# Optimization experiments

Hardware: AMD Instinct MI355X
Metric: run time of the kernel (lower is better)

The kernel has to match this reference:

```python
import jax, jax.numpy as jnp
import numpy as np

B, D, O = 512, 512, 512  # batch, indim, outdim

def setup_inputs() -> dict:
    key = jax.random.key(0)
    k1, k2, k3 = jax.random.split(key, 3)
    x = jax.random.normal(k1, (B, D), dtype=jnp.float32)
    mu_weight = jax.random.normal(k2, (O, D), dtype=jnp.float32) / np.sqrt(D)
    # inverse diagonal covariance entries (positive in spirit; uniform fill)
    inv_diag_C_weight = jax.random.uniform(k3, (O, D), dtype=jnp.float32)
    return {"x": x, "mu_weight": mu_weight, "inv_diag_C_weight": inv_diag_C_weight}

def reference(x, mu_weight, inv_diag_C_weight):
    # Original: logits = -(x-mu) @ diag(invC) @ (x-mu)^T per (batch, class) pair.
    # Diagonal structure => elementwise squared diff weighted by invC, summed over D.
    diff = x[:, None, :] - mu_weight[None, :, :]            # [B, O, D]
    logits = -jnp.einsum('bod,od->bo', diff * diff, inv_diag_C_weight)
    return logits                                            # [B, O]
```

## Files before the change

### kernel.cpp

```cpp
#include <hip/hip_runtime.h>
#include <hip/hip_bf16.h>

#define B_DIM 512
#define D_DIM 512
#define O_DIM 512
#define DCH   128
#define NCH   (D_DIM/DCH)


typedef __attribute__((ext_vector_type(8))) short short8;
typedef __attribute__((ext_vector_type(4))) float f32x4;

__device__ __forceinline__ short f2bf(float f) {
    union { __hip_bfloat16 h; unsigned short u; } cv;
    cv.h = __float2bfloat16(f);
    return (short)cv.u;
}

__global__ __launch_bounds__(256)
void gda_mfma(const float* __restrict__ x,
              const float* __restrict__ mu,
              const float* __restrict__ ic,
              float* __restrict__ out)
{
    __shared__ unsigned short A_lds[32 * 256];
    __shared__ unsigned short B_lds[32 * 256];
    __shared__ float          c_part[32 * 8];
    __shared__ float          c_o[32];

    const int tid = threadIdx.x;
    const int bid = blockIdx.x;
    const int b0 = (bid & 15) * 32;
    const int o0 = (bid >> 4) * 32;

    const int srow = tid >> 3;
    const int su   = tid & 7;

    const int w    = tid >> 6;
    const int lane = tid & 63;
    const int wr   = w >> 1;
    const int wc   = w & 1;
    const int fcol = lane & 15;
    const int fk   = lane >> 4;

    const int rowA = wr * 16 + fcol;
    const int rowB = wc * 16 + fcol;
    const int swA7 = rowA & 7;
    const int swB7 = rowB & 7;

    float creg = 0.0f;
    f32x4 acc = {0.0f, 0.0f, 0.0f, 0.0f};

    for (int ch = 0; ch < NCH; ++ch) {
        const int d0 = ch * DCH;

#pragma unroll
        for (int half = 0; half < 2; ++half) {
            const int uu  = su + half * 8;
            const int swz = uu ^ (srow & 7);
            const int dd  = d0 + uu * 8;

            {
                const float4 p = *(const float4*)&x[(b0 + srow) * D_DIM + dd];
                const float4 q = *(const float4*)&x[(b0 + srow) * D_DIM + dd + 4];
                const float v[8] = {p.x, p.y, p.z, p.w, q.x, q.y, q.z, q.w};
                short8 s2, s1;
#pragma unroll
                for (int e = 0; e < 8; ++e) {
                    s2[e] = f2bf(v[e] * v[e]);
                    s1[e] = f2bf(v[e]);
                }
                *(short8*)&A_lds[(srow * 32 + swz) * 8]      = s2;
                *(short8*)&A_lds[(srow * 32 + 16 + swz) * 8] = s1;
            }
            {
                const int rbase = (o0 + srow) * D_DIM + dd;
                const float4 m0 = *(const float4*)&mu[rbase];
                const float4 m1 = *(const float4*)&mu[rbase + 4];
                const float4 c0 = *(const float4*)&ic[rbase];
                const float4 c1 = *(const float4*)&ic[rbase + 4];
                const float mv[8] = {m0.x, m0.y, m0.z, m0.w, m1.x, m1.y, m1.z, m1.w};
                const float cf[8] = {c0.x, c0.y, c0.z, c0.w, c1.x, c1.y, c1.z, c1.w};
                short8 sa, sb;
#pragma unroll
                for (int e = 0; e < 8; ++e) {
                    sa[e] = f2bf(-cf[e]);
                    sb[e] = f2bf(2.0f * mv[e] * cf[e]);
                    creg  = fmaf(mv[e] * mv[e], cf[e], creg);
                }
                *(short8*)&B_lds[(srow * 32 + swz) * 8]      = sa;
                *(short8*)&B_lds[(srow * 32 + 16 + swz) * 8] = sb;
            }
        }
        __syncthreads();

#pragma unroll
        for (int ks = 0; ks < 8; ++ks) {
            const int g  = ks * 4 + fk;
            const short8 av = *(const short8*)&A_lds[(rowA * 32 + (g ^ swA7)) * 8];
            const short8 bv = *(const short8*)&B_lds[(rowB * 32 + (g ^ swB7)) * 8];
            acc = __builtin_amdgcn_mfma_f32_16x16x32_bf16(av, bv, acc, 0, 0, 0);
        }
        __syncthreads();
    }

    c_part[srow * 8 + su] = creg;
    __syncthreads();
    if (tid < 32) {
        float s = 0.0f;
#pragma unroll
        for (int q = 0; q < 8; ++q) s += c_part[tid * 8 + q];
        c_o[tid] = s;
    }
    __syncthreads();

#pragma unroll
    for (int r = 0; r < 4; ++r) {
        const int row = wr * 16 + fk * 4 + r;
        const int col = wc * 16 + fcol;
        out[(b0 + row) * O_DIM + o0 + col] = acc[r] - c_o[col];
    }
}

extern "C" void kernel_launch(void* const* d_in, const int* in_sizes, int n_in,
                              void* d_out, int out_size, void* d_ws, size_t ws_size,
                              hipStream_t stream) {
    const float* x  = (const float*)d_in[0];
    const float* mu = (const float*)d_in[1];
    const float* ic = (const float*)d_in[2];
    float* out = (float*)d_out;

    gda_mfma<<<dim3(256), dim3(256), 0, stream>>>(x, mu, ic, out);
}
```

Before: 64.14 us.

## Stage full K in LDS once and split K across eight waves

The kernel now loads the whole 512-wide reduction dimension for a 32x32 tile into LDS in one pass with 512 threads, removing the four chunk iterations and their barriers. Each of the eight waves computes the full 32x32 tile over its own K slice using four MFMAs per step. The partial tiles are then reduced through LDS before the bias is subtracted and the result written. LDS use rises sharply, to about 128KB, and the extra cross-wave reduction adds work in exchange for more memory-level parallelism per block.

Result: faster. 62.22 us (-3.0%).

```diff
diff --git a/kernel.cpp b/kernel.cpp
--- a/kernel.cpp
+++ b/kernel.cpp
@@ -4,8 +4,6 @@
 #define B_DIM 512
 #define D_DIM 512
 #define O_DIM 512
-#define DCH   128
-#define NCH   (D_DIM/DCH)
 
 
 typedef __attribute__((ext_vector_type(8))) short short8;
@@ -17,108 +15,130 @@
     return (short)cv.u;
 }
 
-__global__ __launch_bounds__(256)
+__device__ __forceinline__ short8 pack8(float a0, float a1, float a2, float a3,
+                                        float a4, float a5, float a6, float a7) {
+    short8 r;
+    r[0] = f2bf(a0); r[1] = f2bf(a1); r[2] = f2bf(a2); r[3] = f2bf(a3);
+    r[4] = f2bf(a4); r[5] = f2bf(a5); r[6] = f2bf(a6); r[7] = f2bf(a7);
+    return r;
+}
+
+__device__ __forceinline__ int gpos(int g, int row) {
+    return (g & ~15) | ((g & 15) ^ (row & 15));
+}
+
+__global__ __launch_bounds__(512, 2)
 void gda_mfma(const float* __restrict__ x,
               const float* __restrict__ mu,
               const float* __restrict__ ic,
               float* __restrict__ out)
 {
-    __shared__ unsigned short A_lds[32 * 256];
-    __shared__ unsigned short B_lds[32 * 256];
-    __shared__ float          c_part[32 * 8];
-    __shared__ float          c_o[32];
+    __shared__ __align__(16) unsigned short A_lds[32 * 128 * 8];
+    __shared__ __align__(16) unsigned short B_lds[32 * 128 * 8];
+    __shared__ float c_part[512];
+    __shared__ float c_o[32];
 
     const int tid = threadIdx.x;
     const int bid = blockIdx.x;
     const int b0 = (bid & 15) * 32;
     const int o0 = (bid >> 4) * 32;
 
-    const int srow = tid >> 3;
-    const int su   = tid & 7;
+    const int srow = tid >> 4;
+    const int su   = tid & 15;
+
+    float creg = 0.0f;
+#pragma unroll
+    for (int t = 0; t < 4; ++t) {
+        const int g  = su + t * 16;
+        const int dd = g * 8;
+        const float4 p  = *(const float4*)&x [(b0 + srow) * D_DIM + dd];
+        const float4 q  = *(const float4*)&x [(b0 + srow) * D_DIM + dd + 4];
+        const float4 m0 = *(const float4*)&mu[(o0 + srow) * D_DIM + dd];
+        const float4 m1 = *(const float4*)&mu[(o0 + srow) * D_DIM + dd + 4];
+        const float4 c0 = *(const float4*)&ic[(o0 + srow) * D_DIM + dd];
+        const float4 c1 = *(const float4*)&ic[(o0 + srow) * D_DIM + dd + 4];
+
+        const int plo = gpos(g, srow);
+        const int phi = plo + 64;
+
+        *(short8*)&A_lds[(srow * 128 + plo) * 8] =
+            pack8(p.x*p.x, p.y*p.y, p.z*p.z, p.w*p.w,
+                  q.x*q.x, q.y*q.y, q.z*q.z, q.w*q.w);
+        *(short8*)&A_lds[(srow * 128 + phi) * 8] =
+            pack8(p.x, p.y, p.z, p.w, q.x, q.y, q.z, q.w);
+        *(short8*)&B_lds[(srow * 128 + plo) * 8] =
+            pack8(-c0.x, -c0.y, -c0.z, -c0.w, -c1.x, -c1.y, -c1.z, -c1.w);
+        *(short8*)&B_lds[(srow * 128 + phi) * 8] =
+            pack8(2.0f*m0.x*c0.x, 2.0f*m0.y*c0.y, 2.0f*m0.z*c0.z, 2.0f*m0.w*c0.w,
+                  2.0f*m1.x*c1.x, 2.0f*m1.y*c1.y, 2.0f*m1.z*c1.z, 2.0f*m1.w*c1.w);
+
+        creg = fmaf(m0.x*m0.x, c0.x, creg);
+        creg = fmaf(m0.y*m0.y, c0.y, creg);
+        creg = fmaf(m0.z*m0.z, c0.z, creg);
+        creg = fmaf(m0.w*m0.w, c0.w, creg);
+        creg = fmaf(m1.x*m1.x, c1.x, creg);
+        creg = fmaf(m1.y*m1.y, c1.y, creg);
+        creg = fmaf(m1.z*m1.z, c1.z, creg);
+        creg = fmaf(m1.w*m1.w, c1.w, creg);
+    }
+    c_part[tid] = creg;
+    __syncthreads();
+
+    if (tid < 32) {
+        float s = 0.0f;
+#pragma unroll
+        for (int qq = 0; qq < 16; ++qq) s += c_part[tid * 16 + qq];
+        c_o[tid] = s;
+    }
 
     const int w    = tid >> 6;
     const int lane = tid & 63;
-    const int wr   = w >> 1;
-    const int wc   = w & 1;
-    const int fcol = lane & 15;
+    const int fc   = lane & 15;
     const int fk   = lane >> 4;
 
-    const int rowA = wr * 16 + fcol;
-    const int rowB = wc * 16 + fcol;
-    const int swA7 = rowA & 7;
-    const int swB7 = rowB & 7;
-
-    float creg = 0.0f;
-    f32x4 acc = {0.0f, 0.0f, 0.0f, 0.0f};
-
-    for (int ch = 0; ch < NCH; ++ch) {
-        const int d0 = ch * DCH;
+    f32x4 acc[2][2];
+#pragma unroll
+    for (int i = 0; i < 2; ++i)
+#pragma unroll
+        for (int j = 0; j < 2; ++j)
+            acc[i][j] = (f32x4){0.0f, 0.0f, 0.0f, 0.0f};
 
 #pragma unroll
-        for (int half = 0; half < 2; ++half) {
-            const int uu  = su + half * 8;
-            const int swz = uu ^ (srow & 7);
-            const int dd  = d0 + uu * 8;
-
-            {
-                const float4 p = *(const float4*)&x[(b0 + srow) * D_DIM + dd];
-                const float4 q = *(const float4*)&x[(b0 + srow) * D_DIM + dd + 4];
-                const float v[8] = {p.x, p.y, p.z, p.w, q.x, q.y, q.z, q.w};
-                short8 s2, s1;
-#pragma unroll
-                for (int e = 0; e < 8; ++e) {
-                    s2[e] = f2bf(v[e] * v[e]);
-                    s1[e] = f2bf(v[e]);
-                }
-                *(short8*)&A_lds[(srow * 32 + swz) * 8]      = s2;
-                *(short8*)&A_lds[(srow * 32 + 16 + swz) * 8] = s1;
-            }
-            {
-                const int rbase = (o0 + srow) * D_DIM + dd;
-                const float4 m0 = *(const float4*)&mu[rbase];
-                const float4 m1 = *(const float4*)&mu[rbase + 4];
-                const float4 c0 = *(const float4*)&ic[rbase];
-                const float4 c1 = *(const float4*)&ic[rbase + 4];
-                const float mv[8] = {m0.x, m0.y, m0.z, m0.w, m1.x, m1.y, m1.z, m1.w};
-                const float cf[8] = {c0.x, c0.y, c0.z, c0.w, c1.x, c1.y, c1.z, c1.w};
-                short8 sa, sb;
-#pragma unroll
-                for (int e = 0; e < 8; ++e) {
-                    sa[e] = f2bf(-cf[e]);
-                    sb[e] = f2bf(2.0f * mv[e] * cf[e]);
-                    creg  = fmaf(mv[e] * mv[e], cf[e], creg);
-                }
-                *(short8*)&B_lds[(srow * 32 + swz) * 8]      = sa;
-                *(short8*)&B_lds[(srow * 32 + 16 + swz) * 8] = sb;
-            }
-        }
-        __syncthreads();
-
-#pragma unroll
-        for (int ks = 0; ks < 8; ++ks) {
-            const int g  = ks * 4 + fk;
-            const short8 av = *(const short8*)&A_lds[(rowA * 32 + (g ^ swA7)) * 8];
-            const short8 bv = *(const short8*)&B_lds[(rowB * 32 + (g ^ swB7)) * 8];
-            acc = __builtin_amdgcn_mfma_f32_16x16x32_bf16(av, bv, acc, 0, 0, 0);
-        }
-        __syncthreads();
-    }
-
-    c_part[srow * 8 + su] = creg;
-    __syncthreads();
-    if (tid < 32) {
-        float s = 0.0f;
-#pragma unroll
-        for (int q = 0; q < 8; ++q) s += c_part[tid * 8 + q];
-        c_o[tid] = s;
+    for (int m = 0; m < 4; ++m) {
+        const int g = w * 16 + m * 4 + fk;
+        const short8 a0 = *(const short8*)&A_lds[( fc       * 128 + gpos(g, fc     )) * 8];
+        const short8 a1 = *(const short8*)&A_lds[((16 + fc) * 128 + gpos(g, 16 + fc)) * 8];
+        const short8 bv0 = *(const short8*)&B_lds[( fc       * 128 + gpos(g, fc     )) * 8];
+        const short8 bv1 = *(const short8*)&B_lds[((16 + fc) * 128 + gpos(g, 16 + fc)) * 8];
+        acc[0][0] = __builtin_amdgcn_mfma_f32_16x16x32_bf16(a0, bv0, acc[0][0], 0, 0, 0);
+        acc[0][1] = __builtin_amdgcn_mfma_f32_16x16x32_bf16(a0, bv1, acc[0][1], 0, 0, 0);
+        acc[1][0] = __builtin_amdgcn_mfma_f32_16x16x32_bf16(a1, bv0, acc[1][0], 0, 0, 0);
+        acc[1][1] = __builtin_amdgcn_mfma_f32_16x16x32_bf16(a1, bv1, acc[1][1], 0, 0, 0);
     }
     __syncthreads();
 
+    float* part = (float*)A_lds;
 #pragma unroll
-    for (int r = 0; r < 4; ++r) {
-        const int row = wr * 16 + fk * 4 + r;
-        const int col = wc * 16 + fcol;
-        out[(b0 + row) * O_DIM + o0 + col] = acc[r] - c_o[col];
+    for (int i = 0; i < 2; ++i)
+#pragma unroll
+        for (int j = 0; j < 2; ++j)
+#pragma unroll
+            for (int r = 0; r < 4; ++r) {
+                const int lrow = i * 16 + fk * 4 + r;
+                const int lcol = j * 16 + fc;
+                part[w * 1056 + lrow * 33 + lcol] = acc[i][j][r];
+            }
+    __syncthreads();
+
+#pragma unroll
+    for (int p = 0; p < 2; ++p) {
+        const int idx  = p * 512 + tid;
+        const int lrow = idx >> 5;
+        const int lcol = idx & 31;
+        float s = 0.0f;
+#pragma unroll
+        for (int ww = 0; ww < 8; ++ww) s += part[ww * 1056 + lrow * 33 + lcol];
+        out[(b0 + lrow) * O_DIM + o0 + lcol] = s - c_o[lcol];
     }
 }
 
@@ -130,5 +150,5 @@
     const float* ic = (const float*)d_in[2];
     float* out = (float*)d_out;
 
-    gda_mfma<<<dim3(256), dim3(256), 0, stream>>>(x, mu, ic, out);
+    gda_mfma<<<dim3(256), dim3(512), 0, stream>>>(x, mu, ic, out);
 }
```
